# Kernel optimization log

Measured on AMD Instinct MI355X. Metric: run time of the kernel, lower is better.

Reference implementation:

```python
import jax, jax.numpy as jnp
import numpy as np

N_CLASSES = 12
IMG_SIZE = 512
BATCH = 8

CURV_MAX = jnp.array([1.2261, 1.1558, 1.1161, 1.1195, 2.7202, 2.3714,
                      1.7055, 3.2717, 2.6716, 5.0418, 0.4293], dtype=jnp.float32)


def setup_inputs() -> dict:
    key = jax.random.key(0)
    soft_anatomy = jax.random.normal(key, (BATCH, N_CLASSES, IMG_SIZE, IMG_SIZE), dtype=jnp.float32)
    return {"soft_anatomy": soft_anatomy}


def reference(soft_anatomy):
    nc1 = N_CLASSES - 1  # 11 layer channels
    pred_mask = soft_anatomy[:, :nc1]                      # [B, 11, H, W]
    sm = jax.nn.softmax(pred_mask, axis=2)                 # softmax over height (dim 2)
    lsm = jax.nn.log_softmax(pred_mask, axis=2)
    B, C, H, W = sm.shape

    # position mask: row index broadcast over width/channels
    pos = jnp.arange(H, dtype=sm.dtype)[None, None, :, None]  # [1,1,H,1]

    # expected layer position per column: [B, 11, W]
    layer_positions = jnp.sum(sm * pos, axis=2)

    # std deviations around layer positions: [B, 11, W]
    std_deviations = jnp.sqrt(
        jnp.sum(sm * (pos - layer_positions[:, :, None, :]) ** 2, axis=2))

    # topology violations between adjacent layers: [B, 10, W]
    topology_violations = jax.nn.relu(layer_positions[:, :-1] - layer_positions[:, 1:])

    # neighbour (continuity) diff along width: [B, 11, W-1]
    continuity_violations = jnp.abs(
        (jnp.roll(layer_positions, 1, axis=2) - layer_positions)[..., 1:])

    # curvature via depthwise conv1d with sobel [-1,0..0,1] and laplace [1,0..0,-2,0..0,1]
    # (kernel length 11, replicate pad 5 -> same width). torch conv1d is cross-correlation:
    #   first[w]  = -x[w] + x[w+10]
    #   second[w] =  x[w] - 2*x[w+5] + x[w+10]
    PAD = 5
    lpp = jnp.pad(layer_positions, ((0, 0), (0, 0), (PAD, PAD)), mode='edge')
    first_order = lpp[..., 10:] - lpp[..., :-10]
    second_order = lpp[..., :-10] - 2.0 * lpp[..., 5:-5] + lpp[..., 10:]
    curvature = second_order / jnp.power(1.0 + first_order ** 2, 1.5)
    curvature_diffs = jnp.abs(curvature) - CURV_MAX[None, :, None]  # curv_max broadcast over W

    # topological_engine_1d: new[i] = max(new[i-1], lp[i]) == cumulative max over class dim
    correct_layer_positions = jax.lax.cummax(layer_positions, axis=1)

    # cumulative mask: ones channel + cumsum over height -> [B, 12, H, W]
    cum = jnp.cumsum(sm, axis=2)
    ones = jnp.ones((B, 1, H, W), dtype=sm.dtype)
    cm = jnp.concatenate([ones, cum], axis=1)

    # topological_engine_2d: y[idx] = relu(c[idx] + y[idx-1] - 1), idx = 2..n_classes-1
    def step(carry, c):
        y = jax.nn.relu(c + carry - 1.0)
        return y, y

    _, ys = jax.lax.scan(step, cm[:, 1], jnp.moveaxis(cm[:, 2:], 1, 0))
    top_correct = jnp.concatenate([cm[:, :2], jnp.moveaxis(ys, 0, 1)], axis=1)  # [B,12,H,W]

    # separate_masks: forward diff in place; last channel unchanged
    clean_masks = jnp.concatenate(
        [top_correct[:, :-1] - top_correct[:, 1:], top_correct[:, -1:]], axis=1)

    return (lsm, correct_layer_positions, clean_masks,
            std_deviations, topology_violations, continuity_violations, curvature_diffs)
```

## Files before the change

kernel.cpp:

```cpp
#include <hip/hip_runtime.h>

#define BB 8
#define NC 12
#define NC1 11
#define HH 512
#define WW 512
#define NCH 32
#define HC 16
#define NBC (BB*NC1)

static constexpr size_t CH = (size_t)HH * WW;

static constexpr size_t OFF_LSM   = 0;
static constexpr size_t OFF_CLP   = (size_t)BB * NC1 * CH;
static constexpr size_t OFF_CLEAN = OFF_CLP + (size_t)BB * NC1 * WW;
static constexpr size_t OFF_STD   = OFF_CLEAN + (size_t)BB * NC * CH;
static constexpr size_t OFF_TOPO  = OFF_STD + (size_t)BB * NC1 * WW;
static constexpr size_t OFF_CONT  = OFF_TOPO + (size_t)BB * (NC1 - 1) * WW;
static constexpr size_t OFF_CURV  = OFF_CONT + (size_t)BB * NC1 * (WW - 1);

static constexpr size_t WS_E    = 0;
static constexpr size_t WS_P    = (size_t)NBC * NCH * WW;
static constexpr size_t WS_Q    = 2 * WS_P;
static constexpr size_t WS_INV  = 3 * WS_P;
static constexpr size_t WS_LOG  = WS_INV + (size_t)NBC * WW;
static constexpr size_t WS_LP   = WS_LOG + (size_t)NBC * WW;

__global__ __launch_bounds__(512) void k1_partials(const float* __restrict__ in,
                                                   float* __restrict__ ws) {
    const int w4 = threadIdx.x & 127;
    const int cg = threadIdx.x >> 7;
    const int chunk = blockIdx.x * 4 + cg;
    const int bc = blockIdx.y;
    const int b = bc / NC1, c = bc % NC1;

    const float* p = in + ((size_t)(b * NC + c) * HH + (size_t)chunk * HC) * WW + 4 * w4;
    float4 E = make_float4(0.f, 0.f, 0.f, 0.f);
    float4 P = E, Q = E;
#pragma unroll
    for (int i = 0; i < HC; ++i) {
        const float4 x = *(const float4*)(p + (size_t)i * WW);
        const float h = (float)(chunk * HC + i);
        const float ex = expf(x.x), ey = expf(x.y), ez = expf(x.z), ew = expf(x.w);
        E.x += ex; E.y += ey; E.z += ez; E.w += ew;
        P.x += h * ex; P.y += h * ey; P.z += h * ez; P.w += h * ew;
        Q.x += h * h * ex; Q.y += h * h * ey; Q.z += h * h * ez; Q.w += h * h * ew;
    }
    const size_t o = ((size_t)bc * NCH + chunk) * WW + 4 * w4;
    *(float4*)(ws + WS_E + o) = E;
    *(float4*)(ws + WS_P + o) = P;
    *(float4*)(ws + WS_Q + o) = Q;
}

__global__ __launch_bounds__(512) void k2_reduce(float* __restrict__ ws,
                                                 float* __restrict__ out) {
    const int w = threadIdx.x;
    const int bc = blockIdx.x;

    const size_t base0 = (size_t)bc * NCH * WW + w;
    float Ee[NCH];
    float S = 0.f, P = 0.f, Q = 0.f;
#pragma unroll
    for (int k = 0; k < NCH; ++k) {
        const float e = ws[WS_E + base0 + (size_t)k * WW];
        Ee[k] = e;
        S += e;
        P += ws[WS_P + base0 + (size_t)k * WW];
        Q += ws[WS_Q + base0 + (size_t)k * WW];
    }
    const float inv = 1.f / S;
    float pre = 0.f;
#pragma unroll
    for (int k = 0; k < NCH; ++k) {
        ws[WS_E + base0 + (size_t)k * WW] = pre * inv;
        pre += Ee[k];
    }
    const float lp = P * inv;
    float var = Q * inv - lp * lp;
    if (var < 0.f) var = 0.f;

    const size_t o = (size_t)bc * WW + w;
    ws[WS_INV + o] = inv;
    ws[WS_LOG + o] = logf(S);
    ws[WS_LP + o]  = lp;
    out[OFF_STD + o] = sqrtf(var);
}

__global__ __launch_bounds__(256) void k4_main(const float* __restrict__ in,
                                               const float* __restrict__ ws,
                                               float* __restrict__ out) {
    const int t = threadIdx.x;
    const int wh = blockIdx.x, chunk = blockIdx.y, b = blockIdx.z;
    const int w = wh * 256 + t;

    float cum[NC1], inv[NC1], lgs[NC1];
#pragma unroll
    for (int c = 0; c < NC1; ++c) {
        const size_t bc = (size_t)(b * NC1 + c);
        cum[c] = ws[WS_E + (bc * NCH + chunk) * WW + w];
        inv[c] = ws[WS_INV + bc * WW + w];
        lgs[c] = ws[WS_LOG + bc * WW + w];
    }

    const float* ip = in + (size_t)b * NC * CH + (size_t)(chunk * HC) * WW + w;
    float* lsm = out + OFF_LSM + (size_t)b * NC1 * CH + (size_t)(chunk * HC) * WW + w;
    float* cln = out + OFF_CLEAN + (size_t)b * NC * CH + (size_t)(chunk * HC) * WW + w;

    for (int i = 0; i < HC; ++i) {
        const size_t ho = (size_t)i * WW;
        float x[NC1];
#pragma unroll
        for (int c = 0; c < NC1; ++c)
            x[c] = ip[(size_t)c * CH + ho];
#pragma unroll
        for (int c = 0; c < NC1; ++c) {
            cum[c] += expf(x[c]) * inv[c];
            __builtin_nontemporal_store(x[c] - lgs[c], lsm + (size_t)c * CH + ho);
        }
        float tc = cum[0];
        __builtin_nontemporal_store(1.f - tc, cln + ho);
#pragma unroll
        for (int k = 1; k < NC1; ++k) {
            const float t2 = fmaxf(cum[k] + tc - 1.f, 0.f);
            __builtin_nontemporal_store(tc - t2, cln + (size_t)k * CH + ho);
            tc = t2;
        }
        __builtin_nontemporal_store(tc, cln + (size_t)NC1 * CH + ho);
    }

    if (chunk != 0) return;
    const float CM[NC1] = {1.2261f, 1.1558f, 1.1161f, 1.1195f, 2.7202f, 2.3714f,
                           1.7055f, 3.2717f, 2.6716f, 5.0418f, 0.4293f};
    const float* lp = ws + WS_LP;
    const int wm = (w - 5 < 0) ? 0 : w - 5;
    const int wp = (w + 5 > WW - 1) ? WW - 1 : w + 5;
    float m = 0.f, prev = 0.f;
    for (int c = 0; c < NC1; ++c) {
        const size_t rb = (size_t)(b * NC1 + c) * WW;
        const float lv = lp[rb + w];
        m = (c == 0) ? lv : fmaxf(m, lv);
        out[OFF_CLP + rb + w] = m;
        if (c > 0)
            out[OFF_TOPO + (size_t)(b * (NC1 - 1) + (c - 1)) * WW + w] = fmaxf(prev - lv, 0.f);
        prev = lv;
        if (w < WW - 1) {
            const float nxt = lp[rb + w + 1];
            out[OFF_CONT + (size_t)(b * NC1 + c) * (WW - 1) + w] = fabsf(lv - nxt);
        }
        const float a  = lp[rb + wm];
        const float bb = lp[rb + wp];
        const float fo = bb - a;
        const float so = a - 2.f * lv + bb;
        const float bs = 1.f + fo * fo;
        out[OFF_CURV + rb + w] = fabsf(so / (bs * sqrtf(bs))) - CM[c];
    }
}

extern "C" void kernel_launch(void* const* d_in, const int* in_sizes, int n_in,
                              void* d_out, int out_size, void* d_ws, size_t ws_size,
                              hipStream_t stream) {
    const float* in = (const float*)d_in[0];
    float* out = (float*)d_out;
    float* ws = (float*)d_ws;

    hipLaunchKernelGGL(k1_partials, dim3(NCH / 4, NBC), dim3(512), 0, stream, in, ws);
    hipLaunchKernelGGL(k2_reduce, dim3(NBC), dim3(512), 0, stream, ws, out);
    hipLaunchKernelGGL(k4_main, dim3(2, NCH, BB), dim3(256), 0, stream, in, ws, out);
}
```

Measured before the change: 78.40 us.

## Split k2 reduction across chunk quarters with shared-memory combine; use plain stores

The reduction kernel now launches 4x more blocks, each covering 128 columns. Four thread groups each reduce 8 of the 32 height chunks, then combine through shared memory to get totals and per-group prefix offsets. This raises parallelism in a kernel that previously ran only 88 blocks with long serial loops. Separately, the main kernel's nontemporal stores are replaced with ordinary stores, which changes cache behaviour for the large output writes.

```diff
diff --git a/kernel.cpp b/kernel.cpp
--- a/kernel.cpp
+++ b/kernel.cpp
@@ -54,36 +54,50 @@
 
 __global__ __launch_bounds__(512) void k2_reduce(float* __restrict__ ws,
                                                  float* __restrict__ out) {
-    const int w = threadIdx.x;
-    const int bc = blockIdx.x;
+    const int w = threadIdx.x & 127;
+    const int q = threadIdx.x >> 7;
+    const int wt = blockIdx.x;
+    const int bc = blockIdx.y;
+    const int wg = wt * 128 + w;
 
-    const size_t base0 = (size_t)bc * NCH * WW + w;
-    float Ee[NCH];
-    float S = 0.f, P = 0.f, Q = 0.f;
+    __shared__ float sE[4][128], sP[4][128], sQ[4][128];
+
+    const size_t base = (size_t)bc * NCH * WW + wg;
+    float e[8];
+    float Es = 0.f, Ps = 0.f, Qs = 0.f;
 #pragma unroll
-    for (int k = 0; k < NCH; ++k) {
-        const float e = ws[WS_E + base0 + (size_t)k * WW];
-        Ee[k] = e;
-        S += e;
-        P += ws[WS_P + base0 + (size_t)k * WW];
-        Q += ws[WS_Q + base0 + (size_t)k * WW];
+    for (int k = 0; k < 8; ++k) {
+        const int ch = q * 8 + k;
+        e[k] = ws[WS_E + base + (size_t)ch * WW];
+        Es += e[k];
+        Ps += ws[WS_P + base + (size_t)ch * WW];
+        Qs += ws[WS_Q + base + (size_t)ch * WW];
     }
+    sE[q][w] = Es; sP[q][w] = Ps; sQ[q][w] = Qs;
+    __syncthreads();
+
+    const float S = sE[0][w] + sE[1][w] + sE[2][w] + sE[3][w];
     const float inv = 1.f / S;
     float pre = 0.f;
+    for (int q2 = 0; q2 < q; ++q2) pre += sE[q2][w];
 #pragma unroll
-    for (int k = 0; k < NCH; ++k) {
-        ws[WS_E + base0 + (size_t)k * WW] = pre * inv;
-        pre += Ee[k];
+    for (int k = 0; k < 8; ++k) {
+        const int ch = q * 8 + k;
+        ws[WS_E + base + (size_t)ch * WW] = pre * inv;
+        pre += e[k];
     }
-    const float lp = P * inv;
-    float var = Q * inv - lp * lp;
-    if (var < 0.f) var = 0.f;
-
-    const size_t o = (size_t)bc * WW + w;
-    ws[WS_INV + o] = inv;
-    ws[WS_LOG + o] = logf(S);
-    ws[WS_LP + o]  = lp;
-    out[OFF_STD + o] = sqrtf(var);
+    if (q == 0) {
+        const float P = sP[0][w] + sP[1][w] + sP[2][w] + sP[3][w];
+        const float Q = sQ[0][w] + sQ[1][w] + sQ[2][w] + sQ[3][w];
+        const float lp = P * inv;
+        float var = Q * inv - lp * lp;
+        if (var < 0.f) var = 0.f;
+        const size_t o = (size_t)bc * WW + wg;
+        ws[WS_INV + o] = inv;
+        ws[WS_LOG + o] = logf(S);
+        ws[WS_LP + o]  = lp;
+        out[OFF_STD + o] = sqrtf(var);
+    }
 }
 
 __global__ __launch_bounds__(256) void k4_main(const float* __restrict__ in,
@@ -115,17 +129,17 @@
 #pragma unroll
         for (int c = 0; c < NC1; ++c) {
             cum[c] += expf(x[c]) * inv[c];
-            __builtin_nontemporal_store(x[c] - lgs[c], lsm + (size_t)c * CH + ho);
+            lsm[(size_t)c * CH + ho] = x[c] - lgs[c];
         }
         float tc = cum[0];
-        __builtin_nontemporal_store(1.f - tc, cln + ho);
+        cln[ho] = 1.f - tc;
 #pragma unroll
         for (int k = 1; k < NC1; ++k) {
             const float t2 = fmaxf(cum[k] + tc - 1.f, 0.f);
-            __builtin_nontemporal_store(tc - t2, cln + (size_t)k * CH + ho);
+            cln[(size_t)k * CH + ho] = tc - t2;
             tc = t2;
         }
-        __builtin_nontemporal_store(tc, cln + (size_t)NC1 * CH + ho);
+        cln[(size_t)NC1 * CH + ho] = tc;
     }
 
     if (chunk != 0) return;
@@ -164,6 +178,6 @@
     float* ws = (float*)d_ws;
 
     hipLaunchKernelGGL(k1_partials, dim3(NCH / 4, NBC), dim3(512), 0, stream, in, ws);
-    hipLaunchKernelGGL(k2_reduce, dim3(NBC), dim3(512), 0, stream, ws, out);
+    hipLaunchKernelGGL(k2_reduce, dim3(4, NBC), dim3(512), 0, stream, ws, out);
     hipLaunchKernelGGL(k4_main, dim3(2, NCH, BB), dim3(256), 0, stream, in, ws, out);
 }
```

After: 78.46 us. No clear change (+0.1%).
